# Optimization experiments

Hardware: AMD Instinct MI355X
Metric: run time of the kernel (lower is better)

## Reference

```python
import jax, jax.numpy as jnp
import numpy as np

STATE_DIM = 16
CHANNELS = 256
LENGTH = 8192
SAMPLE_RATE = 100.0


def setup_inputs() -> dict:
    key = jax.random.key(0)
    ks = jax.random.split(key, 4)
    fan = 1.0 / np.sqrt(CHANNELS)  # lecun-normal-ish scale, flax Dense default
    x = jax.random.normal(ks[0], (LENGTH, CHANNELS), dtype=jnp.float32)
    logA = jnp.log(1.0 + jnp.arange(STATE_DIM, dtype=jnp.float32))  # module's Ainit
    W_dt = jax.random.normal(ks[1], (CHANNELS, CHANNELS), dtype=jnp.float32) * fan
    b_dt = jnp.zeros((CHANNELS,), dtype=jnp.float32)
    W_B = jax.random.normal(ks[2], (CHANNELS, STATE_DIM), dtype=jnp.float32) * fan
    b_B = jnp.zeros((STATE_DIM,), dtype=jnp.float32)
    W_C = jax.random.normal(ks[3], (CHANNELS, STATE_DIM), dtype=jnp.float32) * fan
    b_C = jnp.zeros((STATE_DIM,), dtype=jnp.float32)
    return {"x": x, "logA": logA, "W_dt": W_dt, "b_dt": b_dt,
            "W_B": W_B, "b_B": b_B, "W_C": W_C, "b_C": b_C}


def reference(x, logA, W_dt, b_dt, W_B, b_B, W_C, b_C):
    # x: (L, C)
    A = -jnp.exp(logA)                                   # (S,)
    dt = jax.nn.softplus(1.0 / SAMPLE_RATE + x @ W_dt + b_dt)  # (L, C)
    B = 1.0 + x @ W_B + b_B                              # (L, S)
    C = x @ W_C + b_C                                    # (L, S)
    # discretize: Adiscr = exp(A * dt), shape (L, C, S)
    Adiscr = jnp.exp(dt[:, :, None] * A[None, None, :])
    # Bdiscr = exp((Adiscr - 1) * (B / A))  (faithful to source, incl. outer exp)
    Bdiscr = jnp.exp((Adiscr - 1.0) * (B / A)[:, None, :])  # (L, C, S)
    u = Bdiscr * x[:, :, None]                           # (L, C, S)

    def ssm_scan(p1, p2):
        (A1, c1), (A2, c2) = p1, p2
        return (A2 * A1, c2 + A2 * c1)

    _, h = jax.lax.associative_scan(ssm_scan, (Adiscr, u))  # h: (L, C, S)
    y = jnp.einsum('ls,lcs->lc', C, h)                    # (L, C)
    return y
```

## Files before the change

kernel.cpp:

```cpp
#include <hip/hip_runtime.h>
#include <hip/hip_bf16.h>
#include <math.h>

#define LL 8192
#define CC 256
#define SS 16
#define NJ (CC*SS)
#define GG 256
#define TT 32
#define THREADS 512
#define SEGS 16
#define PER (GG/SEGS)
#define SP 4
#define CB 64

#define LOG2E 1.4426950408889634f
#define LN2   0.6931471805599453f

#define XSTR 264
#define WSTR 264
#define DSTR 260

typedef __attribute__((ext_vector_type(8))) short short8;
typedef __attribute__((ext_vector_type(4))) float floatx4;

__device__ __forceinline__ float fexp2(float v){ return __builtin_amdgcn_exp2f(v); }
__device__ __forceinline__ float flog2v(float v){ return __builtin_amdgcn_logf(v); }

__device__ __forceinline__ float softplus(float z){
    float t = fexp2(-fabsf(z) * LOG2E);
    return fmaxf(z, 0.f) + LN2 * flog2v(1.f + t);
}

__device__ __forceinline__ unsigned short f2b(float f){
    __hip_bfloat16 h = __float2bfloat16(f);
    return *(unsigned short*)&h;
}
__device__ __forceinline__ float b2f(unsigned short u){
    __hip_bfloat16 h = *(__hip_bfloat16*)&u;
    return __bfloat162float(h);
}

__global__ __launch_bounds__(THREADS, 2) void k_mmscan(
    const float* __restrict__ x, const float* __restrict__ logA,
    const float* __restrict__ Wdt, const float* __restrict__ bdt,
    const float* __restrict__ WB,  const float* __restrict__ bB,
    const float* __restrict__ WC,  const float* __restrict__ bC,
    float* __restrict__ dt, float* __restrict__ boa, float* __restrict__ cm,
    float* __restrict__ Ap, float* __restrict__ Hl)
{
    __shared__ unsigned short xh[32*XSTR];
    __shared__ unsigned short xl[32*XSTR];
    __shared__ unsigned short Wh2[64*WSTR];
    __shared__ unsigned short Wl2[64*WSTR];
    __shared__ float dtS[32*DSTR];
    __shared__ float boaS[32*SS];
    __shared__ float cmS[32*SS];

    const int tid  = threadIdx.x;
    const int g    = blockIdx.x;
    const int row0 = g * TT;

    #pragma unroll
    for (int j = 0; j < 4; j++){
        int idx = tid + j*THREADS;
        int r   = idx >> 6;
        int kq  = (idx & 63) * 4;
        float4 f = *(const float4*)&x[(size_t)(row0+r)*CC + kq];
        float fv[4] = {f.x, f.y, f.z, f.w};
        unsigned short hs[4], ls[4];
        #pragma unroll
        for (int i=0;i<4;i++){ hs[i]=f2b(fv[i]); ls[i]=f2b(fv[i]-b2f(hs[i])); }
        uint2 ph, pl;
        ph.x = (unsigned)hs[0] | ((unsigned)hs[1] << 16);
        ph.y = (unsigned)hs[2] | ((unsigned)hs[3] << 16);
        pl.x = (unsigned)ls[0] | ((unsigned)ls[1] << 16);
        pl.y = (unsigned)ls[2] | ((unsigned)ls[3] << 16);
        *(uint2*)&xh[r*XSTR + kq] = ph;
        *(uint2*)&xl[r*XSTR + kq] = pl;
    }

    const int lane = tid & 63;
    const int wv   = tid >> 6;
    const int m16  = lane & 15;
    const int q    = lane >> 4;
    const int mi   = wv & 1;
    const int ni   = wv >> 1;

    const int cw = tid & 63;
    const int kb = (tid >> 6) * 32;

    for (int nt = 0; nt < 5; nt++){
        {
            int bcol = nt*64 + cw;
            const float* wp = nullptr; int wstr = 0;
            if (bcol < 256)      { wp = Wdt + bcol;       wstr = CC; }
            else if (bcol < 272) { wp = WB  + (bcol-256); wstr = SS; }
            else if (bcol < 288) { wp = WC  + (bcol-272); wstr = SS; }
            if (wp){
                #pragma unroll
                for (int i8 = 0; i8 < 32; i8 += 8){
                    unsigned short hs[8], ls[8];
                    #pragma unroll
                    for (int u = 0; u < 8; u++){
                        float v = wp[(size_t)(kb+i8+u)*wstr];
                        hs[u] = f2b(v);
                        ls[u] = f2b(v - b2f(hs[u]));
                    }
                    uint4 ph, pl;
                    ph.x = (unsigned)hs[0] | ((unsigned)hs[1] << 16);
                    ph.y = (unsigned)hs[2] | ((unsigned)hs[3] << 16);
                    ph.z = (unsigned)hs[4] | ((unsigned)hs[5] << 16);
                    ph.w = (unsigned)hs[6] | ((unsigned)hs[7] << 16);
                    pl.x = (unsigned)ls[0] | ((unsigned)ls[1] << 16);
                    pl.y = (unsigned)ls[2] | ((unsigned)ls[3] << 16);
                    pl.z = (unsigned)ls[4] | ((unsigned)ls[5] << 16);
                    pl.w = (unsigned)ls[6] | ((unsigned)ls[7] << 16);
                    *(uint4*)&Wh2[cw*WSTR + kb + i8] = ph;
                    *(uint4*)&Wl2[cw*WSTR + kb + i8] = pl;
                }
            }
        }
        __syncthreads();

        if (nt < 4 || ni < 2){
            floatx4 acc = (floatx4){0.f,0.f,0.f,0.f};
            #pragma unroll
            for (int ks = 0; ks < 256; ks += 32){
                short8 bh = *(const short8*)&Wh2[(ni*16+m16)*WSTR + ks + q*8];
                short8 bl = *(const short8*)&Wl2[(ni*16+m16)*WSTR + ks + q*8];
                short8 ah = *(const short8*)&xh [(mi*16+m16)*XSTR + ks + q*8];
                short8 al = *(const short8*)&xl [(mi*16+m16)*XSTR + ks + q*8];
                acc = __builtin_amdgcn_mfma_f32_16x16x32_bf16(al, bh, acc, 0, 0, 0);
                acc = __builtin_amdgcn_mfma_f32_16x16x32_bf16(ah, bl, acc, 0, 0, 0);
                acc = __builtin_amdgcn_mfma_f32_16x16x32_bf16(ah, bh, acc, 0, 0, 0);
            }
            int col   = nt*64 + ni*16 + m16;
            int rbase = mi*16 + q*4;
            if (col < 256){
                float bias = bdt[col];
                #pragma unroll
                for (int r=0;r<4;r++){
                    float v = softplus(0.01f + acc[r] + bias);
                    dtS[(rbase+r)*DSTR + col] = v;
                    dt[(size_t)(row0+rbase+r)*CC + col] = v;
                }
            } else if (col < 272){
                int s = col - 256;
                float A  = -fexp2(logA[s]*LOG2E);
                float sc = LOG2E / A;
                float bias = bB[s];
                #pragma unroll
                for (int r=0;r<4;r++){
                    float v = (1.f + acc[r] + bias) * sc;
                    boaS[(rbase+r)*SS + s] = v;
                    boa[(size_t)(row0+rbase+r)*SS + s] = v;
                }
            } else {
                int s = col - 272;
                float bias = bC[s];
                #pragma unroll
                for (int r=0;r<4;r++){
                    float v = acc[r] + bias;
                    cmS[(rbase+r)*SS + s] = v;
                    cm[(size_t)(row0+rbase+r)*SS + s] = v;
                }
            }
        }
        __syncthreads();
    }

    const int c  = tid >> 1;
    const int sb = (tid & 1) * 8;

    float Al2v[8];
    #pragma unroll
    for (int i=0;i<8;i++) Al2v[i] = -fexp2(logA[sb+i]*LOG2E) * LOG2E;

    const float* __restrict__ xp = x + (size_t)row0*CC + c;

    float Apr[8], h[8];
    #pragma unroll
    for (int i=0;i<8;i++){ Apr[i]=1.f; h[i]=0.f; }

    #pragma unroll 8
    for (int t=0;t<TT;t++){
        float d  = dtS[t*DSTR + c];
        float xv = xp[(size_t)t*CC];
        float4 b0 = *(const float4*)&boaS[t*SS + sb];
        float4 b1 = *(const float4*)&boaS[t*SS + sb + 4];
        float bo[8] = {b0.x,b0.y,b0.z,b0.w,b1.x,b1.y,b1.z,b1.w};
        #pragma unroll
        for (int s=0;s<8;s++){
            float a = fexp2(d * Al2v[s]);
            float u = fexp2(fmaf(a, bo[s], -bo[s])) * xv;
            h[s] = fmaf(a, h[s], u);
            Apr[s] *= a;
        }
    }
    {
        const size_t base = (size_t)g*NJ + (size_t)c*SS + sb;
        *(float4*)&Ap[base]   = make_float4(Apr[0],Apr[1],Apr[2],Apr[3]);
        *(float4*)&Ap[base+4] = make_float4(Apr[4],Apr[5],Apr[6],Apr[7]);
        *(float4*)&Hl[base]   = make_float4(h[0],h[1],h[2],h[3]);
        *(float4*)&Hl[base+4] = make_float4(h[4],h[5],h[6],h[7]);
    }
}

__global__ __launch_bounds__(256) void k_carry(const float* __restrict__ Ap,
    const float* __restrict__ Hl, float* __restrict__ Cr)
{
    const int tid = threadIdx.x;
    const int jl  = tid & 15;
    const int seg = tid >> 4;
    const int j   = blockIdx.x * 16 + jl;

    const size_t base = (size_t)(seg*PER)*NJ + j;

    float a[PER], u[PER];
    #pragma unroll
    for (int k=0;k<PER;k++){
        a[k] = Ap[base + (size_t)k*NJ];
        u[k] = Hl[base + (size_t)k*NJ];
    }
    float Aag = 1.f, Uag = 0.f;
    #pragma unroll
    for (int k=0;k<PER;k++){ Uag = fmaf(a[k], Uag, u[k]); Aag *= a[k]; }

    __shared__ float As[SEGS][17], Us[SEGS][17];
    As[seg][jl] = Aag; Us[seg][jl] = Uag;
    __syncthreads();
    float hin = 0.f;
    for (int t = 0; t < seg; ++t)
        hin = fmaf(As[t][jl], hin, Us[t][jl]);

    float h = hin;
    #pragma unroll
    for (int k=0;k<PER;k++){
        Cr[base + (size_t)k*NJ] = h;
        h = fmaf(a[k], h, u[k]);
    }
}

__global__ __launch_bounds__(256) void k_scan2(const float* __restrict__ dt,
    const float* __restrict__ x, const float* __restrict__ boa,
    const float* __restrict__ cmat, const float* __restrict__ logA,
    const float* __restrict__ Cr, float* __restrict__ y)
{
    const int tid = threadIdx.x;
    const int sg  = tid & 3;
    const int cl  = tid >> 2;
    const int g   = blockIdx.x;
    const int c   = blockIdx.y * CB + cl;
    const int row0 = g * TT;

    float Al2[SP];
    #pragma unroll
    for (int i=0;i<SP;i++) Al2[i] = -fexp2(logA[sg*SP+i]*LOG2E) * LOG2E;

    const float* __restrict__ dp = dt   + (size_t)row0*CC + c;
    const float* __restrict__ xp = x    + (size_t)row0*CC + c;
    const float* __restrict__ bp = boa  + (size_t)row0*SS + sg*SP;
    const float* __restrict__ cp = cmat + (size_t)row0*SS + sg*SP;
    float* __restrict__ yp = y + (size_t)row0*CC + c;

    float h[SP];
    {
        float4 hc = *(const float4*)&Cr[(size_t)g*NJ + (size_t)c*SS + sg*SP];
        h[0]=hc.x; h[1]=hc.y; h[2]=hc.z; h[3]=hc.w;
    }

    #pragma unroll 8
    for (int t=0;t<TT;t++){
        float d  = dp[(size_t)t*CC];
        float xv = xp[(size_t)t*CC];
        float4 bo = *(const float4*)&bp[(size_t)t*SS];
        float4 cv = *(const float4*)&cp[(size_t)t*SS];
        float bov[SP] = {bo.x,bo.y,bo.z,bo.w};
        float cvv[SP] = {cv.x,cv.y,cv.z,cv.w};
        float yv = 0.f;
        #pragma unroll
        for (int s=0;s<SP;s++){
            float a = fexp2(d * Al2[s]);
            float u = fexp2(fmaf(a, bov[s], -bov[s])) * xv;
            h[s] = fmaf(a, h[s], u);
            yv = fmaf(cvv[s], h[s], yv);
        }
        yv += __shfl_xor(yv, 1);
        yv += __shfl_xor(yv, 2);
        if (sg == 0) yp[(size_t)t*CC] = yv;
    }
}

extern "C" void kernel_launch(void* const* d_in, const int* in_sizes, int n_in,
                              void* d_out, int out_size, void* d_ws, size_t ws_size,
                              hipStream_t stream) {
    const float* x    = (const float*)d_in[0];
    const float* logA = (const float*)d_in[1];
    const float* W_dt = (const float*)d_in[2];
    const float* b_dt = (const float*)d_in[3];
    const float* W_B  = (const float*)d_in[4];
    const float* b_B  = (const float*)d_in[5];
    const float* W_C  = (const float*)d_in[6];
    const float* b_C  = (const float*)d_in[7];
    float* y  = (float*)d_out;
    float* ws = (float*)d_ws;

    float* dt   = ws;
    float* boa  = dt   + (size_t)LL*CC;
    float* cmv  = boa  + (size_t)LL*SS;
    float* Ap   = cmv  + (size_t)LL*SS;
    float* Hl   = Ap   + (size_t)GG*NJ;
    float* Cr   = Hl   + (size_t)GG*NJ;

    hipLaunchKernelGGL(k_mmscan, dim3(GG), dim3(THREADS), 0, stream,
                       x, logA, W_dt, b_dt, W_B, b_B, W_C, b_C,
                       dt, boa, cmv, Ap, Hl);
    hipLaunchKernelGGL(k_carry, dim3(NJ/16), dim3(256), 0, stream, Ap, Hl, Cr);
    hipLaunchKernelGGL(k_scan2, dim3(GG,4), dim3(256), 0, stream,
                       dt, x, boa, cmv, logA, Cr, y);
}
```

Baseline: 119.7 us.

## Precompute split-bf16 weights once and halve time tile to double block count

Adds a prep kernel that converts W_dt/W_B/W_C to transposed hi/lo bf16 arrays once, so the fused matmul+scan kernel reads pre-split weights from global/L2 instead of each block re-converting them into shared memory. The time tile drops from 32 to 16 rows, giving 512 blocks with smaller LDS and a higher occupancy target. This removes redundant per-block weight conversion and barriers, at the cost of an extra launch, more carry entries for the cross-block scan, and MFMA B-operands fetched directly from global memory.

```diff
diff --git a/kernel.cpp b/kernel.cpp
--- a/kernel.cpp
+++ b/kernel.cpp
@@ -6,20 +6,20 @@
 #define CC 256
 #define SS 16
 #define NJ (CC*SS)
-#define GG 256
-#define TT 32
+#define GG 512
+#define TT 16
 #define THREADS 512
 #define SEGS 16
 #define PER (GG/SEGS)
 #define SP 4
 #define CB 64
+#define NCOL 288
 
 #define LOG2E 1.4426950408889634f
 #define LN2   0.6931471805599453f
 
 #define XSTR 264
-#define WSTR 264
-#define DSTR 260
+#define DSTR 264
 
 typedef __attribute__((ext_vector_type(8))) short short8;
 typedef __attribute__((ext_vector_type(4))) float floatx4;
@@ -41,28 +41,42 @@
     return __bfloat162float(h);
 }
 
-__global__ __launch_bounds__(THREADS, 2) void k_mmscan(
+__global__ __launch_bounds__(256) void k_prep(
+    const float* __restrict__ Wdt, const float* __restrict__ WB,
+    const float* __restrict__ WC,
+    unsigned short* __restrict__ Wh, unsigned short* __restrict__ Wl)
+{
+    const int col = blockIdx.x;
+    const int k   = threadIdx.x;
+    float v;
+    if (col < 256)      v = Wdt[(size_t)k*CC + col];
+    else if (col < 272) v = WB [(size_t)k*SS + (col-256)];
+    else                v = WC [(size_t)k*SS + (col-272)];
+    unsigned short h = f2b(v);
+    Wh[(size_t)col*CC + k] = h;
+    Wl[(size_t)col*CC + k] = f2b(v - b2f(h));
+}
+
+__global__ __launch_bounds__(THREADS, 4) void k_mmscan(
     const float* __restrict__ x, const float* __restrict__ logA,
-    const float* __restrict__ Wdt, const float* __restrict__ bdt,
-    const float* __restrict__ WB,  const float* __restrict__ bB,
-    const float* __restrict__ WC,  const float* __restrict__ bC,
+    const unsigned short* __restrict__ Whg, const unsigned short* __restrict__ Wlg,
+    const float* __restrict__ bdt, const float* __restrict__ bB,
+    const float* __restrict__ bC,
     float* __restrict__ dt, float* __restrict__ boa, float* __restrict__ cm,
     float* __restrict__ Ap, float* __restrict__ Hl)
 {
-    __shared__ unsigned short xh[32*XSTR];
-    __shared__ unsigned short xl[32*XSTR];
-    __shared__ unsigned short Wh2[64*WSTR];
-    __shared__ unsigned short Wl2[64*WSTR];
-    __shared__ float dtS[32*DSTR];
-    __shared__ float boaS[32*SS];
-    __shared__ float cmS[32*SS];
+    __shared__ unsigned short xh[16*XSTR];
+    __shared__ unsigned short xl[16*XSTR];
+    __shared__ float dtS[16*DSTR];
+    __shared__ float boaS[16*SS];
+    __shared__ float cmS[16*SS];
 
     const int tid  = threadIdx.x;
     const int g    = blockIdx.x;
     const int row0 = g * TT;
 
     #pragma unroll
-    for (int j = 0; j < 4; j++){
+    for (int j = 0; j < 2; j++){
         int idx = tid + j*THREADS;
         int r   = idx >> 6;
         int kq  = (idx & 63) * 4;
@@ -84,91 +98,56 @@
     const int wv   = tid >> 6;
     const int m16  = lane & 15;
     const int q    = lane >> 4;
-    const int mi   = wv & 1;
-    const int ni   = wv >> 1;
-
-    const int cw = tid & 63;
-    const int kb = (tid >> 6) * 32;
-
-    for (int nt = 0; nt < 5; nt++){
-        {
-            int bcol = nt*64 + cw;
-            const float* wp = nullptr; int wstr = 0;
-            if (bcol < 256)      { wp = Wdt + bcol;       wstr = CC; }
-            else if (bcol < 272) { wp = WB  + (bcol-256); wstr = SS; }
-            else if (bcol < 288) { wp = WC  + (bcol-272); wstr = SS; }
-            if (wp){
-                #pragma unroll
-                for (int i8 = 0; i8 < 32; i8 += 8){
-                    unsigned short hs[8], ls[8];
-                    #pragma unroll
-                    for (int u = 0; u < 8; u++){
-                        float v = wp[(size_t)(kb+i8+u)*wstr];
-                        hs[u] = f2b(v);
-                        ls[u] = f2b(v - b2f(hs[u]));
-                    }
-                    uint4 ph, pl;
-                    ph.x = (unsigned)hs[0] | ((unsigned)hs[1] << 16);
-                    ph.y = (unsigned)hs[2] | ((unsigned)hs[3] << 16);
-                    ph.z = (unsigned)hs[4] | ((unsigned)hs[5] << 16);
-                    ph.w = (unsigned)hs[6] | ((unsigned)hs[7] << 16);
-                    pl.x = (unsigned)ls[0] | ((unsigned)ls[1] << 16);
-                    pl.y = (unsigned)ls[2] | ((unsigned)ls[3] << 16);
-                    pl.z = (unsigned)ls[4] | ((unsigned)ls[5] << 16);
-                    pl.w = (unsigned)ls[6] | ((unsigned)ls[7] << 16);
-                    *(uint4*)&Wh2[cw*WSTR + kb + i8] = ph;
-                    *(uint4*)&Wl2[cw*WSTR + kb + i8] = pl;
-                }
+
+    __syncthreads();
+
+    for (int ct = wv; ct < 18; ct += 8){
+        const int col = ct*16 + m16;
+        const unsigned short* __restrict__ WhP = Whg + (size_t)col*CC + q*8;
+        const unsigned short* __restrict__ WlP = Wlg + (size_t)col*CC + q*8;
+        floatx4 acc = (floatx4){0.f,0.f,0.f,0.f};
+        #pragma unroll
+        for (int ks = 0; ks < 256; ks += 32){
+            short8 bh = *(const short8*)&WhP[ks];
+            short8 bl = *(const short8*)&WlP[ks];
+            short8 ah = *(const short8*)&xh[m16*XSTR + ks + q*8];
+            short8 al = *(const short8*)&xl[m16*XSTR + ks + q*8];
+            acc = __builtin_amdgcn_mfma_f32_16x16x32_bf16(al, bh, acc, 0, 0, 0);
+            acc = __builtin_amdgcn_mfma_f32_16x16x32_bf16(ah, bl, acc, 0, 0, 0);
+            acc = __builtin_amdgcn_mfma_f32_16x16x32_bf16(ah, bh, acc, 0, 0, 0);
+        }
+        const int rbase = q*4;
+        if (col < 256){
+            float bias = bdt[col];
+            #pragma unroll
+            for (int r=0;r<4;r++){
+                float v = softplus(0.01f + acc[r] + bias);
+                dtS[(rbase+r)*DSTR + col] = v;
+                dt[(size_t)(row0+rbase+r)*CC + col] = v;
+            }
+        } else if (col < 272){
+            int s = col - 256;
+            float A  = -fexp2(logA[s]*LOG2E);
+            float sc = LOG2E / A;
+            float bias = bB[s];
+            #pragma unroll
+            for (int r=0;r<4;r++){
+                float v = (1.f + acc[r] + bias) * sc;
+                boaS[(rbase+r)*SS + s] = v;
+                boa[(size_t)(row0+rbase+r)*SS + s] = v;
+            }
+        } else {
+            int s = col - 272;
+            float bias = bC[s];
+            #pragma unroll
+            for (int r=0;r<4;r++){
+                float v = acc[r] + bias;
+                cmS[(rbase+r)*SS + s] = v;
+                cm[(size_t)(row0+rbase+r)*SS + s] = v;
             }
         }
-        __syncthreads();
-
-        if (nt < 4 || ni < 2){
-            floatx4 acc = (floatx4){0.f,0.f,0.f,0.f};
-            #pragma unroll
-            for (int ks = 0; ks < 256; ks += 32){
-                short8 bh = *(const short8*)&Wh2[(ni*16+m16)*WSTR + ks + q*8];
-                short8 bl = *(const short8*)&Wl2[(ni*16+m16)*WSTR + ks + q*8];
-                short8 ah = *(const short8*)&xh [(mi*16+m16)*XSTR + ks + q*8];
-                short8 al = *(const short8*)&xl [(mi*16+m16)*XSTR + ks + q*8];
-                acc = __builtin_amdgcn_mfma_f32_16x16x32_bf16(al, bh, acc, 0, 0, 0);
-                acc = __builtin_amdgcn_mfma_f32_16x16x32_bf16(ah, bl, acc, 0, 0, 0);
-                acc = __builtin_amdgcn_mfma_f32_16x16x32_bf16(ah, bh, acc, 0, 0, 0);
-            }
-            int col   = nt*64 + ni*16 + m16;
-            int rbase = mi*16 + q*4;
-            if (col < 256){
-                float bias = bdt[col];
-                #pragma unroll
-                for (int r=0;r<4;r++){
-                    float v = softplus(0.01f + acc[r] + bias);
-                    dtS[(rbase+r)*DSTR + col] = v;
-                    dt[(size_t)(row0+rbase+r)*CC + col] = v;
-                }
-            } else if (col < 272){
-                int s = col - 256;
-                float A  = -fexp2(logA[s]*LOG2E);
-                float sc = LOG2E / A;
-                float bias = bB[s];
-                #pragma unroll
-                for (int r=0;r<4;r++){
-                    float v = (1.f + acc[r] + bias) * sc;
-                    boaS[(rbase+r)*SS + s] = v;
-                    boa[(size_t)(row0+rbase+r)*SS + s] = v;
-                }
-            } else {
-                int s = col - 272;
-                float bias = bC[s];
-                #pragma unroll
-                for (int r=0;r<4;r++){
-                    float v = acc[r] + bias;
-                    cmS[(rbase+r)*SS + s] = v;
-                    cm[(size_t)(row0+rbase+r)*SS + s] = v;
-                }
-            }
-        }
-        __syncthreads();
-    }
+    }
+    __syncthreads();
 
     const int c  = tid >> 1;
     const int sb = (tid & 1) * 8;
@@ -312,9 +291,13 @@
     float* Ap   = cmv  + (size_t)LL*SS;
     float* Hl   = Ap   + (size_t)GG*NJ;
     float* Cr   = Hl   + (size_t)GG*NJ;
-
+    unsigned short* Wh = (unsigned short*)(Cr + (size_t)GG*NJ);
+    unsigned short* Wl = Wh + (size_t)NCOL*CC;
+
+    hipLaunchKernelGGL(k_prep, dim3(NCOL), dim3(256), 0, stream,
+                       W_dt, W_B, W_C, Wh, Wl);
     hipLaunchKernelGGL(k_mmscan, dim3(GG), dim3(THREADS), 0, stream,
-                       x, logA, W_dt, b_dt, W_B, b_B, W_C, b_C,
+                       x, logA, Wh, Wl, b_dt, b_B, b_C,
                        dt, boa, cmv, Ap, Hl);
     hipLaunchKernelGGL(k_carry, dim3(NJ/16), dim3(256), 0, stream, Ap, Hl, Cr);
     hipLaunchKernelGGL(k_scan2, dim3(GG,4), dim3(256), 0, stream,
```

Measured after the change: 127.8 us. 6.7% more time.
